# Performance work log

Hardware: AMD Instinct MI355X
Metric: run time of the kernel (lower is better)

Reference implementation:

```python
import jax, jax.numpy as jnp
from jax import lax
import numpy as np

B, T = 32, 64
E = 64        # embed_dim
U = 32        # num_measurements
D0, D1 = 300, 100
S = 9         # speaker_num
CELL = 64     # output_cell_dim
C = 6         # n_classes
EPS = 1e-12


def setup_inputs() -> dict:
    key = jax.random.key(0)
    ks = jax.random.split(key, 16)
    sc = 1.0 / np.sqrt(E)
    n = lambda i, shape, s=1.0: (jax.random.normal(ks[i], shape, jnp.float32) * s)
    return {
        "x0": n(0, (B, T, D0)),
        "x1": n(1, (B, T, D1)),
        "smask": jax.random.uniform(ks[2], (B, T, S), jnp.float32),
        "umask": jnp.ones((B, T), jnp.float32),
        "W_ih0": n(3, (4 * E, D0), sc), "W_hh0": n(4, (4 * E, E), sc),
        "b_ih0": n(5, (4 * E,), sc), "b_hh0": n(6, (4 * E,), sc),
        "W_ih1": n(7, (4 * E, D1), sc), "W_hh1": n(8, (4 * E, E), sc),
        "b_ih1": n(9, (4 * E,), sc), "b_hh1": n(10, (4 * E,), sc),
        "phase_table": jax.random.uniform(ks[11], (S, E), jnp.float32, -np.pi, np.pi),
        "meas_kernel": jax.random.uniform(ks[12], (U, E, 2), jnp.float32),
        "W1": n(13, (CELL, 2 * U), 0.1), "b1": jnp.zeros((CELL,), jnp.float32),
        "W2": n(14, (C, CELL), 0.1), "b2": jnp.zeros((C,), jnp.float32),
    }


def _lstm_tanh(x, um, Wih, Whh, bih, bhh):
    # torch.nn.LSTMCell (gate order i,f,g,o) + extra tanh applied to h each step;
    # the tanh-ed h is carried as the recurrent state (dropout = identity in eval).
    b, t, _ = x.shape
    e = Whh.shape[1]

    def step(carry, inp):
        h, c = carry
        xt, ut = inp
        g = (xt * ut[:, None]) @ Wih.T + bih + h @ Whh.T + bhh
        i, f, gg, o = jnp.split(g, 4, axis=-1)
        c = jax.nn.sigmoid(f) * c + jax.nn.sigmoid(i) * jnp.tanh(gg)
        h = jnp.tanh(jax.nn.sigmoid(o) * jnp.tanh(c))
        return (h, c), h

    h0 = jnp.zeros((b, e), x.dtype)
    _, hs = lax.scan(step, (h0, h0), (jnp.swapaxes(x, 0, 1), um.T))
    return jnp.swapaxes(hs, 0, 1)  # (B,T,E)


def _measure(amp, phase, kernel):
    # pure state v = cos(phase)*amp + i sin(phase)*amp; rho = |v><v|
    r = jnp.cos(phase) * amp
    im = jnp.sin(phase) * amp
    rho_r = jnp.einsum('bti,btj->btij', r, r) + jnp.einsum('bti,btj->btij', im, im)
    rho_i = jnp.einsum('bti,btj->btij', im, r) - jnp.einsum('bti,btj->btij', r, im)
    u = kernel.shape[0]
    norm = jnp.clip(jnp.linalg.norm(kernel.reshape(u, -1), axis=-1), EPS)
    kn = kernel / norm[:, None, None]
    kr, ki = kn[..., 0], kn[..., 1]
    Pr = jnp.einsum('ui,uj->uij', kr, kr) + jnp.einsum('ui,uj->uij', ki, ki)
    Pi = jnp.einsum('ui,uj->uij', ki, kr) - jnp.einsum('ui,uj->uij', kr, ki)
    return jnp.einsum('btij,uij->btu', rho_r, Pr) - jnp.einsum('btij,uij->btu', rho_i, Pi)


def reference(x0, x1, smask, umask, W_ih0, W_hh0, b_ih0, b_hh0,
              W_ih1, W_hh1, b_ih1, b_hh1, phase_table, meas_kernel,
              W1, b1, W2, b2):
    h0 = _lstm_tanh(x0, umask, W_ih0, W_hh0, b_ih0, b_hh0)
    h1 = _lstm_tanh(x1, umask, W_ih1, W_hh1, b_ih1, b_hh1)
    norm = lambda h: h / jnp.clip(jnp.linalg.norm(h, axis=-1, keepdims=True), EPS)
    phase = phase_table[jnp.argmax(smask, axis=-1)]  # (B,T,E); table shared by both modalities
    m = jnp.concatenate([_measure(norm(h0), phase, meas_kernel),
                         _measure(norm(h1), phase, meas_kernel)], axis=-1)
    hid = jax.nn.relu(m @ W1.T + b1)
    pred = jnp.tanh(hid @ W2.T + b2)
    return jax.nn.log_softmax(pred, axis=2)
```

## Files before the change

kernel.cpp:

```cpp
#include <hip/hip_runtime.h>

typedef unsigned short ushort_t;
typedef unsigned int uint_t;
typedef float f32x2 __attribute__((ext_vector_type(2)));

__device__ __forceinline__ float bf2f(ushort_t v) {
  union { uint_t u; float f; } x; x.u = ((uint_t)v) << 16; return x.f;
}
__device__ __forceinline__ float lo16(uint_t u) {
  union { uint_t u; float f; } x; x.u = u << 16; return x.f;
}
__device__ __forceinline__ float hi16(uint_t u) {
  union { uint_t u; float f; } x; x.u = u & 0xffff0000u; return x.f;
}
__device__ __forceinline__ ushort_t f2bf(float f) {
  union { float f; uint_t u; } x; x.f = f;
  uint_t u = x.u;
  uint_t r = (u + 0x7fffu + ((u >> 16) & 1u)) >> 16;
  return (ushort_t)r;
}
__device__ __forceinline__ bool is_bf16(const void* um) {
  return *(const uint_t*)um == 0x3F803F80u;
}
__device__ __forceinline__ float ld_dual(const void* p, int i, bool isb) {
  return isb ? bf2f(((const ushort_t*)p)[i]) : ((const float*)p)[i];
}
__device__ __forceinline__ float fsig(float x) { return 1.f / (1.f + __expf(-x)); }
__device__ __forceinline__ float ftanh(float x) { return 2.f / (1.f + __expf(-2.f * x)) - 1.f; }

#if defined(__has_builtin)
#if __has_builtin(__builtin_elementwise_fma)
#define FMA2(a, b, c) __builtin_elementwise_fma((a), (b), (c))
#endif
#endif
#ifndef FMA2
__device__ __forceinline__ f32x2 fma2_fb(f32x2 a, f32x2 b, f32x2 c) {
  c.x = fmaf(a.x, b.x, c.x); c.y = fmaf(a.y, b.y, c.y); return c;
}
#define FMA2(a, b, c) fma2_fb((a), (b), (c))
#endif

__device__ __forceinline__ float dpp_add_xor1(float v) {
  const int r = __builtin_amdgcn_update_dpp(0, __float_as_int(v), 0xB1, 0xF, 0xF, true);
  return v + __int_as_float(r);
}
__device__ __forceinline__ float dpp_add_xor2(float v) {
  const int r = __builtin_amdgcn_update_dpp(0, __float_as_int(v), 0x4E, 0xF, 0xF, true);
  return v + __int_as_float(r);
}

template <int D, bool ISB>
__device__ __forceinline__ void proj_body(
    const void* __restrict__ x, const void* __restrict__ um,
    const void* __restrict__ Wih, const void* __restrict__ bih,
    const void* __restrict__ bhh, float* __restrict__ xw, float* xs)
{
  const int tid = threadIdx.x;
  const int gp = tid & 127;
  const int rg4 = (tid >> 7) << 2;
  const int r0 = blockIdx.x * 16;
  for (int i = tid; i < 16 * D; i += 512) {
    const int r = i / D;
    xs[i] = ld_dual(x, r0 * D + i, ISB) * ld_dual(um, r0 + r, ISB);
  }
  __syncthreads();
  f32x2 acc[2][4];
#pragma unroll
  for (int g = 0; g < 2; ++g)
#pragma unroll
    for (int r = 0; r < 4; ++r) acc[g][r] = f32x2{0.f, 0.f};
#pragma unroll 5
  for (int k = 0; k < D; k += 4) {
    f32x2 wA0, wA1, wB0, wB1;
    if (ISB) {
      const ushort_t* w0p = (const ushort_t*)Wih + (2 * gp) * D + k;
      const uint2 u0 = *(const uint2*)w0p;
      const uint2 u1 = *(const uint2*)(w0p + D);
      wA0 = f32x2{lo16(u0.x), hi16(u0.x)}; wA1 = f32x2{lo16(u0.y), hi16(u0.y)};
      wB0 = f32x2{lo16(u1.x), hi16(u1.x)}; wB1 = f32x2{lo16(u1.y), hi16(u1.y)};
    } else {
      const float* w0p = (const float*)Wih + (2 * gp) * D + k;
      const float4 f0 = *(const float4*)w0p;
      const float4 f1 = *(const float4*)(w0p + D);
      wA0 = f32x2{f0.x, f0.y}; wA1 = f32x2{f0.z, f0.w};
      wB0 = f32x2{f1.x, f1.y}; wB1 = f32x2{f1.z, f1.w};
    }
#pragma unroll
    for (int r = 0; r < 4; ++r) {
      const float4 xv = *(const float4*)(xs + (rg4 + r) * D + k);
      const f32x2 xA = {xv.x, xv.y}, xB = {xv.z, xv.w};
      acc[0][r] = FMA2(xA, wA0, acc[0][r]);
      acc[0][r] = FMA2(xB, wA1, acc[0][r]);
      acc[1][r] = FMA2(xA, wB0, acc[1][r]);
      acc[1][r] = FMA2(xB, wB1, acc[1][r]);
    }
  }
  const int g0 = 2 * gp, g1 = 2 * gp + 1;
  const float b0 = ld_dual(bih, g0, ISB) + ld_dual(bhh, g0, ISB);
  const float b1v = ld_dual(bih, g1, ISB) + ld_dual(bhh, g1, ISB);
  const int pos0 = ((g0 & 63) << 2) | (g0 >> 6);
  const int pos1 = ((g1 & 63) << 2) | (g1 >> 6);
#pragma unroll
  for (int r = 0; r < 4; ++r) {
    const int row = r0 + rg4 + r;
    xw[row * 256 + pos0] = acc[0][r].x + acc[0][r].y + b0;
    xw[row * 256 + pos1] = acc[1][r].x + acc[1][r].y + b1v;
  }
}

__global__ __launch_bounds__(512) void proj_both(
    const void* __restrict__ x0, const void* __restrict__ x1,
    const void* __restrict__ um,
    const void* __restrict__ Wih0, const void* __restrict__ bih0,
    const void* __restrict__ bhh0,
    const void* __restrict__ Wih1, const void* __restrict__ bih1,
    const void* __restrict__ bhh1,
    float* __restrict__ xw0, float* __restrict__ xw1)
{
  __shared__ __align__(16) float xs[16 * 300];
  const bool isb = is_bf16(um);
  if (blockIdx.y == 0) {
    if (isb) proj_body<300, true>(x0, um, Wih0, bih0, bhh0, xw0, xs);
    else     proj_body<300, false>(x0, um, Wih0, bih0, bhh0, xw0, xs);
  } else {
    if (isb) proj_body<100, true>(x1, um, Wih1, bih1, bhh1, xw1, xs);
    else     proj_body<100, false>(x1, um, Wih1, bih1, bhh1, xw1, xs);
  }
}

__global__ __launch_bounds__(256, 1) void lstm_k(
    const float* __restrict__ xw0, const float* __restrict__ xw1,
    const void* __restrict__ Whh0, const void* __restrict__ Whh1,
    const void* __restrict__ um,
    float* __restrict__ h0r, float* __restrict__ h1r)
{
  __shared__ __align__(16) float xws[64 * 256];
  __shared__ __align__(16) float hist[65 * 64];

  const int bid = blockIdx.x;
  const int l = bid >> 5;
  const int b = bid & 31;
  const float* xw = (l ? xw1 : xw0) + b * 64 * 256;
  const void* Whh = (l ? Whh1 : Whh0);
  float* hr = (l ? h1r : h0r) + b * 64 * 64;
  const int tid = threadIdx.x;
  const int e = tid >> 2;
  const int q = tid & 3;
  const int k0 = q << 4;
  const bool isb = is_bf16(um);

  for (int i = tid; i < 4096; i += 256)
    *(float4*)(xws + i * 4) = *(const float4*)(xw + i * 4);
  if (tid < 64) hist[tid] = 0.f;

  f32x2 w2[4][8];
  if (isb) {
#pragma unroll
    for (int t = 0; t < 4; ++t) {
      const ushort_t* wr = (const ushort_t*)Whh + (t * 64 + e) * 64 + k0;
#pragma unroll
      for (int j = 0; j < 16; j += 8) {
        const uint4 v = *(const uint4*)(wr + j);
        w2[t][(j >> 1) + 0] = f32x2{lo16(v.x), hi16(v.x)};
        w2[t][(j >> 1) + 1] = f32x2{lo16(v.y), hi16(v.y)};
        w2[t][(j >> 1) + 2] = f32x2{lo16(v.z), hi16(v.z)};
        w2[t][(j >> 1) + 3] = f32x2{lo16(v.w), hi16(v.w)};
      }
    }
  } else {
#pragma unroll
    for (int t = 0; t < 4; ++t) {
      const float* wr = (const float*)Whh + (t * 64 + e) * 64 + k0;
#pragma unroll
      for (int j = 0; j < 16; j += 4) {
        const float4 v = *(const float4*)(wr + j);
        w2[t][(j >> 1) + 0] = f32x2{v.x, v.y};
        w2[t][(j >> 1) + 1] = f32x2{v.z, v.w};
      }
    }
  }
  __syncthreads();

  float c = 0.f;
  for (int s = 0; s < 64; ++s) {
    const float gin = xws[s * 256 + tid];
    const float* hp = hist + s * 64 + k0;
    f32x2 P0 = {0.f, 0.f}, P1 = {0.f, 0.f}, P2 = {0.f, 0.f}, P3 = {0.f, 0.f};
#pragma unroll
    for (int j = 0; j < 16; j += 4) {
      const float4 hv = *(const float4*)(hp + j);
      const f32x2 hA = {hv.x, hv.y}, hB = {hv.z, hv.w};
      const int jp = j >> 1;
      P0 = FMA2(w2[0][jp], hA, P0); P0 = FMA2(w2[0][jp + 1], hB, P0);
      P1 = FMA2(w2[1][jp], hA, P1); P1 = FMA2(w2[1][jp + 1], hB, P1);
      P2 = FMA2(w2[2][jp], hA, P2); P2 = FMA2(w2[2][jp + 1], hB, P2);
      P3 = FMA2(w2[3][jp], hA, P3); P3 = FMA2(w2[3][jp + 1], hB, P3);
    }
    float p0 = P0.x + P0.y;
    float p1 = P1.x + P1.y;
    float p2 = P2.x + P2.y;
    float p3 = P3.x + P3.y;
    if (q == 0) p0 += gin;
    else if (q == 1) p1 += gin;
    else if (q == 2) p2 += gin;
    else p3 += gin;
    p0 = dpp_add_xor1(p0); p0 = dpp_add_xor2(p0);
    p1 = dpp_add_xor1(p1); p1 = dpp_add_xor2(p1);
    p2 = dpp_add_xor1(p2); p2 = dpp_add_xor2(p2);
    p3 = dpp_add_xor1(p3); p3 = dpp_add_xor2(p3);
    const float yi = fsig(p0);
    const float yf = fsig(p1);
    const float yg = ftanh(p2);
    const float yo = fsig(p3);
    c = fmaf(yf, c, yi * yg);
    const float h = ftanh(yo * ftanh(c));
    if (q == 0) hist[(s + 1) * 64 + e] = h;
    __syncthreads();
  }
  for (int i = tid; i < 1024; i += 256)
    *(float4*)(hr + i * 4) = *(const float4*)(hist + 64 + i * 4);
}

__global__ __launch_bounds__(256) void head_k(
    const float* __restrict__ h0r, const float* __restrict__ h1r,
    const void* __restrict__ smask, const void* __restrict__ um,
    const void* __restrict__ ptab, const void* __restrict__ mker,
    const void* __restrict__ W1, const void* __restrict__ b1,
    const void* __restrict__ W2, const void* __restrict__ b2,
    void* __restrict__ out)
{
  __shared__ float2 knT[64][32];
  __shared__ float w1T[64][65];
  __shared__ float w2T[64][9];
  __shared__ float b1s[64];
  __shared__ float b2s[8];
  __shared__ float rim[4][4][64];
  __shared__ float msh[4][64];
  __shared__ float hidsh[4][64];
  __shared__ float psh[4][8];

  const int tid = threadIdx.x;
  const bool isb = is_bf16(um);
  {
    const int u = tid >> 3, sub = tid & 7;
    float vr[8], vi[8];
    float ssq = 0.f;
#pragma unroll
    for (int qq = 0; qq < 8; ++qq) {
      const int e = sub * 8 + qq;
      if (isb) {
        const uint_t kk = ((const uint_t*)mker)[u * 64 + e];
        vr[qq] = lo16(kk); vi[qq] = hi16(kk);
      } else {
        const float2 kk = ((const float2*)mker)[u * 64 + e];
        vr[qq] = kk.x; vi[qq] = kk.y;
      }
      ssq = fmaf(vr[qq], vr[qq], ssq);
      ssq = fmaf(vi[qq], vi[qq], ssq);
    }
    ssq += __shfl_xor(ssq, 1);
    ssq += __shfl_xor(ssq, 2);
    ssq += __shfl_xor(ssq, 4);
    const float rn = 1.f / fmaxf(sqrtf(ssq), 1e-12f);
#pragma unroll
    for (int qq = 0; qq < 8; ++qq) {
      const int e = sub * 8 + qq;
      knT[e][u] = make_float2(vr[qq] * rn, vi[qq] * rn);
    }
  }
  for (int i = tid; i < 4096; i += 256) {
    const int j = i >> 6, ll = i & 63;
    w1T[ll][j] = ld_dual(W1, i, isb);
  }
  if (tid < 64) b1s[tid] = ld_dual(b1, tid, isb);
  for (int i = tid; i < 384; i += 256) {
    const int cc = i >> 6, j = i & 63;
    w2T[j][cc] = ld_dual(W2, i, isb);
  }
  if (tid < 6) b2s[tid] = ld_dual(b2, tid, isb);
  __syncthreads();

  const int wv = tid >> 6, lane = tid & 63;
  const int item = blockIdx.x * 4 + wv;
  const float h0raw = h0r[item * 64 + lane];
  const float h1raw = h1r[item * 64 + lane];
  float ss0 = h0raw * h0raw, ss1 = h1raw * h1raw;
#pragma unroll
  for (int m = 1; m < 64; m <<= 1) {
    ss0 += __shfl_xor(ss0, m);
    ss1 += __shfl_xor(ss1, m);
  }
  const float h0 = h0raw / fmaxf(sqrtf(ss0), 1e-12f);
  const float h1 = h1raw / fmaxf(sqrtf(ss1), 1e-12f);

  int idx = 0;
  if (lane == 0) {
    float best = -1e30f;
#pragma unroll
    for (int si = 0; si < 9; ++si) {
      const float v = ld_dual(smask, item * 9 + si, isb);
      if (v > best) { best = v; idx = si; }
    }
  }
  idx = __shfl(idx, 0, 64);
  const float ph = ld_dual(ptab, idx * 64 + lane, isb);
  float sr, cr;
  __sincosf(ph, &sr, &cr);
  rim[wv][0][lane] = cr * h0;
  rim[wv][1][lane] = sr * h0;
  rim[wv][2][lane] = cr * h1;
  rim[wv][3][lane] = sr * h1;
  __syncthreads();
  {
    const int u = lane & 31;
    const float* ra = rim[wv][(lane >= 32) ? 2 : 0];
    const float* ia = rim[wv][(lane >= 32) ? 3 : 1];
    float ar = 0.f, ai = 0.f;
#pragma unroll 8
    for (int e = 0; e < 64; ++e) {
      const float2 k = knT[e][u];
      const float rr = ra[e], ii = ia[e];
      ar = fmaf(rr, k.x, ar);
      ar = fmaf(-ii, k.y, ar);
      ai = fmaf(rr, k.y, ai);
      ai = fmaf(ii, k.x, ai);
    }
    msh[wv][lane] = fmaf(ar, ar, ai * ai);
  }
  __syncthreads();
  {
    float acc = b1s[lane];
#pragma unroll 8
    for (int L = 0; L < 64; ++L)
      acc = fmaf(msh[wv][L], w1T[L][lane], acc);
    hidsh[wv][lane] = fmaxf(acc, 0.f);
  }
  __syncthreads();
  if (lane < 6) {
    float a2 = b2s[lane];
#pragma unroll 8
    for (int j = 0; j < 64; ++j)
      a2 = fmaf(hidsh[wv][j], w2T[j][lane], a2);
    psh[wv][lane] = ftanh(a2);
  }
  __syncthreads();
  if (lane < 6) {
    const float p = psh[wv][lane];
    float mx = psh[wv][0];
#pragma unroll
    for (int cc = 1; cc < 6; ++cc) mx = fmaxf(mx, psh[wv][cc]);
    float sum = 0.f;
#pragma unroll
    for (int cc = 0; cc < 6; ++cc) sum += __expf(psh[wv][cc] - mx);
    const float res = p - mx - __logf(sum);
    if (isb) ((ushort_t*)out)[item * 6 + lane] = f2bf(res);
    else     ((float*)out)[item * 6 + lane] = res;
  }
}

extern "C" void kernel_launch(void* const* d_in, const int* in_sizes, int n_in,
                              void* d_out, int out_size, void* d_ws, size_t ws_size,
                              hipStream_t stream)
{
  (void)in_sizes; (void)n_in; (void)out_size; (void)ws_size;
  const void* x0    = d_in[0];
  const void* x1    = d_in[1];
  const void* smask = d_in[2];
  const void* um    = d_in[3];
  const void* Wih0  = d_in[4];
  const void* Whh0  = d_in[5];
  const void* bih0  = d_in[6];
  const void* bhh0  = d_in[7];
  const void* Wih1  = d_in[8];
  const void* Whh1  = d_in[9];
  const void* bih1  = d_in[10];
  const void* bhh1  = d_in[11];
  const void* ptab  = d_in[12];
  const void* mker  = d_in[13];
  const void* W1    = d_in[14];
  const void* b1    = d_in[15];
  const void* W2    = d_in[16];
  const void* b2    = d_in[17];

  float* xw0 = (float*)d_ws;
  float* xw1 = xw0 + 2048 * 256;
  float* h0r = xw1 + 2048 * 256;
  float* h1r = h0r + 2048 * 64;

  hipLaunchKernelGGL(proj_both, dim3(128, 2), dim3(512), 0, stream,
                     x0, x1, um, Wih0, bih0, bhh0, Wih1, bih1, bhh1,
                     xw0, xw1);
  hipLaunchKernelGGL(lstm_k, dim3(64), dim3(256), 0, stream,
                     xw0, xw1, Whh0, Whh1, um, h0r, h1r);
  hipLaunchKernelGGL(head_k, dim3(512), dim3(256), 0, stream,
                     h0r, h1r, smask, um, ptab, mker, W1, b1, W2, b2,
                     d_out);
}
```

Measured before the change: 174.6 us.

## Simplify input projection to one gate per thread with direct global reads

The input projection kernel drops its shared-memory staging of x and the paired-gate FMA2 tiling. Each of 256 threads now computes one gate column for 4 rows, reading x straight from global memory, and the grid grows from 128 to 512 blocks per modality. The umask multiply moves to the epilogue and is applied to the accumulated dot product. This gives more blocks and removes the barrier, but costs less register reuse of weights, more redundant global or L1 reads of x across threads, and scalar FMAs instead of packed ones.

Result: slower. 181.2 us (+3.8%).

```diff
diff --git a/kernel.cpp b/kernel.cpp
--- a/kernel.cpp
+++ b/kernel.cpp
@@ -53,62 +53,49 @@
 __device__ __forceinline__ void proj_body(
     const void* __restrict__ x, const void* __restrict__ um,
     const void* __restrict__ Wih, const void* __restrict__ bih,
-    const void* __restrict__ bhh, float* __restrict__ xw, float* xs)
-{
-  const int tid = threadIdx.x;
-  const int gp = tid & 127;
-  const int rg4 = (tid >> 7) << 2;
-  const int r0 = blockIdx.x * 16;
-  for (int i = tid; i < 16 * D; i += 512) {
-    const int r = i / D;
-    xs[i] = ld_dual(x, r0 * D + i, ISB) * ld_dual(um, r0 + r, ISB);
-  }
-  __syncthreads();
-  f32x2 acc[2][4];
-#pragma unroll
-  for (int g = 0; g < 2; ++g)
-#pragma unroll
-    for (int r = 0; r < 4; ++r) acc[g][r] = f32x2{0.f, 0.f};
-#pragma unroll 5
+    const void* __restrict__ bhh, float* __restrict__ xw)
+{
+  const int g = threadIdx.x;
+  const int r0 = blockIdx.x * 4;
+  float acc[4] = {0.f, 0.f, 0.f, 0.f};
+  const float* xf = (const float*)x;
+  const ushort_t* xh = (const ushort_t*)x;
+#pragma unroll 2
   for (int k = 0; k < D; k += 4) {
-    f32x2 wA0, wA1, wB0, wB1;
+    float w0, w1, w2, w3;
     if (ISB) {
-      const ushort_t* w0p = (const ushort_t*)Wih + (2 * gp) * D + k;
-      const uint2 u0 = *(const uint2*)w0p;
-      const uint2 u1 = *(const uint2*)(w0p + D);
-      wA0 = f32x2{lo16(u0.x), hi16(u0.x)}; wA1 = f32x2{lo16(u0.y), hi16(u0.y)};
-      wB0 = f32x2{lo16(u1.x), hi16(u1.x)}; wB1 = f32x2{lo16(u1.y), hi16(u1.y)};
+      const uint2 wu = *(const uint2*)((const ushort_t*)Wih + g * D + k);
+      w0 = lo16(wu.x); w1 = hi16(wu.x); w2 = lo16(wu.y); w3 = hi16(wu.y);
     } else {
-      const float* w0p = (const float*)Wih + (2 * gp) * D + k;
-      const float4 f0 = *(const float4*)w0p;
-      const float4 f1 = *(const float4*)(w0p + D);
-      wA0 = f32x2{f0.x, f0.y}; wA1 = f32x2{f0.z, f0.w};
-      wB0 = f32x2{f1.x, f1.y}; wB1 = f32x2{f1.z, f1.w};
+      const float4 wv = *(const float4*)((const float*)Wih + g * D + k);
+      w0 = wv.x; w1 = wv.y; w2 = wv.z; w3 = wv.w;
     }
 #pragma unroll
     for (int r = 0; r < 4; ++r) {
-      const float4 xv = *(const float4*)(xs + (rg4 + r) * D + k);
-      const f32x2 xA = {xv.x, xv.y}, xB = {xv.z, xv.w};
-      acc[0][r] = FMA2(xA, wA0, acc[0][r]);
-      acc[0][r] = FMA2(xB, wA1, acc[0][r]);
-      acc[1][r] = FMA2(xA, wB0, acc[1][r]);
-      acc[1][r] = FMA2(xB, wB1, acc[1][r]);
-    }
-  }
-  const int g0 = 2 * gp, g1 = 2 * gp + 1;
-  const float b0 = ld_dual(bih, g0, ISB) + ld_dual(bhh, g0, ISB);
-  const float b1v = ld_dual(bih, g1, ISB) + ld_dual(bhh, g1, ISB);
-  const int pos0 = ((g0 & 63) << 2) | (g0 >> 6);
-  const int pos1 = ((g1 & 63) << 2) | (g1 >> 6);
+      float xa, xb, xc, xd;
+      if (ISB) {
+        const uint2 xu = *(const uint2*)(xh + (r0 + r) * D + k);
+        xa = lo16(xu.x); xb = hi16(xu.x); xc = lo16(xu.y); xd = hi16(xu.y);
+      } else {
+        const float4 xv = *(const float4*)(xf + (r0 + r) * D + k);
+        xa = xv.x; xb = xv.y; xc = xv.z; xd = xv.w;
+      }
+      acc[r] = fmaf(xa, w0, acc[r]);
+      acc[r] = fmaf(xb, w1, acc[r]);
+      acc[r] = fmaf(xc, w2, acc[r]);
+      acc[r] = fmaf(xd, w3, acc[r]);
+    }
+  }
+  const float bias = ld_dual(bih, g, ISB) + ld_dual(bhh, g, ISB);
+  const int pos = ((g & 63) << 2) | (g >> 6);
 #pragma unroll
   for (int r = 0; r < 4; ++r) {
-    const int row = r0 + rg4 + r;
-    xw[row * 256 + pos0] = acc[0][r].x + acc[0][r].y + b0;
-    xw[row * 256 + pos1] = acc[1][r].x + acc[1][r].y + b1v;
-  }
-}
-
-__global__ __launch_bounds__(512) void proj_both(
+    const float u = ld_dual(um, r0 + r, ISB);
+    xw[(r0 + r) * 256 + pos] = fmaf(acc[r], u, bias);
+  }
+}
+
+__global__ __launch_bounds__(256) void proj_both(
     const void* __restrict__ x0, const void* __restrict__ x1,
     const void* __restrict__ um,
     const void* __restrict__ Wih0, const void* __restrict__ bih0,
@@ -117,14 +104,13 @@
     const void* __restrict__ bhh1,
     float* __restrict__ xw0, float* __restrict__ xw1)
 {
-  __shared__ __align__(16) float xs[16 * 300];
   const bool isb = is_bf16(um);
   if (blockIdx.y == 0) {
-    if (isb) proj_body<300, true>(x0, um, Wih0, bih0, bhh0, xw0, xs);
-    else     proj_body<300, false>(x0, um, Wih0, bih0, bhh0, xw0, xs);
+    if (isb) proj_body<300, true>(x0, um, Wih0, bih0, bhh0, xw0);
+    else     proj_body<300, false>(x0, um, Wih0, bih0, bhh0, xw0);
   } else {
-    if (isb) proj_body<100, true>(x1, um, Wih1, bih1, bhh1, xw1, xs);
-    else     proj_body<100, false>(x1, um, Wih1, bih1, bhh1, xw1, xs);
+    if (isb) proj_body<100, true>(x1, um, Wih1, bih1, bhh1, xw1);
+    else     proj_body<100, false>(x1, um, Wih1, bih1, bhh1, xw1);
   }
 }
 
@@ -387,7 +373,7 @@
   float* h0r = xw1 + 2048 * 256;
   float* h1r = h0r + 2048 * 64;
 
-  hipLaunchKernelGGL(proj_both, dim3(128, 2), dim3(512), 0, stream,
+  hipLaunchKernelGGL(proj_both, dim3(512, 2), dim3(256), 0, stream,
                      x0, x1, um, Wih0, bih0, bhh0, Wih1, bih1, bhh1,
                      xw0, xw1);
   hipLaunchKernelGGL(lstm_k, dim3(64), dim3(256), 0, stream,
```
